# Kernel optimization log

Hardware: AMD Instinct MI355X
Metric: run time of the kernel (lower is better)

## Reference

```python
import jax, jax.numpy as jnp
import numpy as np

B, NN, D, H, L, E, NC = 512, 64, 128, 4, 2, 262144, 8
N = B * NN
HD = D // H


def _mlp(x, W1, b1, W2, b2):
    return jax.nn.relu(x @ W1 + b1) @ W2 + b2


def setup_inputs() -> dict:
    key = jax.random.key(0)
    ks = iter(jax.random.split(key, 64))
    w = lambda shape, s=0.02: jax.random.normal(next(ks), shape, dtype=jnp.float32) * s
    inp = {
        'node_features': jax.random.randint(next(ks), (N,), 0, NC, dtype=jnp.int32),
        'edge_index': jax.random.randint(next(ks), (2, E), 0, N, dtype=jnp.int32),
        'ptr': jnp.arange(B + 1, dtype=jnp.int32) * NN,
        'node_emb_table': w((NC, D), 1.0),
        'edge_emb': jnp.clip(jax.random.normal(next(ks), (1, D), dtype=jnp.float32), -2.0, 2.0),
        'eW1': w((L, 3 * D, D)), 'eb1': jnp.zeros((L, D)), 'eW2': w((L, D, D)), 'eb2': jnp.zeros((L, D)),
        'nW1': w((L, 3 * D, D)), 'nb1': jnp.zeros((L, D)), 'nW2': w((L, D, D)), 'nb2': jnp.zeros((L, D)),
        'gW1': w((L, 3 * D, D)), 'gb1': jnp.zeros((L, D)), 'gW2': w((L, D, D)), 'gb2': jnp.zeros((L, D)),
        'projW': w((D, 3 * D)), 'projb': jnp.zeros((3 * D,)),
        'Wq': w((D, D)), 'Wk': w((D, D)), 'Wv': w((D, D)),
        'bq': jnp.zeros((D,)), 'bk': jnp.zeros((D,)), 'bv': jnp.zeros((D,)),
        'outW': w((D, D)), 'outb': jnp.zeros((D,)),
        'sW1': w((D, D)), 'sb1': jnp.zeros((D,)), 'sW2': w((D, D)), 'sb2': jnp.zeros((D,)),
        'rW1': w((D, D)), 'rb1': jnp.zeros((D,)), 'rW2': w((D, D)), 'rb2': jnp.zeros((D,)),
        'stW1': w((D, D)), 'stb1': jnp.zeros((D,)), 'stW2': w((D, 1)), 'stb2': jnp.zeros((1,)),
        'temperature': jnp.float32(1.0),
    }
    return inp


def reference(node_features, edge_index, ptr, node_emb_table, edge_emb,
              eW1, eb1, eW2, eb2, nW1, nb1, nW2, nb2, gW1, gb1, gW2, gb2,
              projW, projb, Wq, Wk, Wv, bq, bk, bv, outW, outb,
              sW1, sb1, sW2, sb2, rW1, rb1, rW2, rb2,
              stW1, stb1, stW2, stb2, temperature):
    n_graphs = ptr.shape[0] - 1                       # static
    batch_idx = jnp.repeat(jnp.arange(n_graphs), NN)  # uniform graphs of NN nodes
    node_embs = node_emb_table[node_features]         # [N, D]
    edge_embs = jnp.broadcast_to(edge_emb, (edge_index.shape[1], D))  # [E, D]
    g = jnp.zeros((n_graphs, D), node_embs.dtype)
    src, dst = edge_index[0], edge_index[1]
    for l in range(L):
        ein = jnp.concatenate([node_embs[src], node_embs[dst], edge_embs], -1)  # [E, 3D]
        edge_embs = edge_embs + _mlp(ein, eW1[l], eb1[l], eW2[l], eb2[l])
        node_aggr = jax.ops.segment_sum(edge_embs, dst, num_segments=N)         # [N, D]
        nin = jnp.concatenate([node_embs, node_aggr, g[batch_idx]], -1)
        node_embs = node_embs + _mlp(nin, nW1[l], nb1[l], nW2[l], nb2[l])
        eg = jax.ops.segment_sum(node_aggr, batch_idx, num_segments=n_graphs)
        ng = jax.ops.segment_sum(node_embs, batch_idx, num_segments=n_graphs)
        g = g + _mlp(jnp.concatenate([ng, eg, g], -1), gW1[l], gb1[l], gW2[l], gb2[l])
    # projection + self-attention over the NN nodes of each graph
    x = node_embs.reshape(n_graphs, NN, D) @ projW + projb   # [B, NN, 3D]
    q, k, v = jnp.split(x, 3, axis=-1)
    qh = (q @ Wq + bq).reshape(n_graphs, NN, H, HD)
    kh = (k @ Wk + bk).reshape(n_graphs, NN, H, HD)
    vh = (v @ Wv + bv).reshape(n_graphs, NN, H, HD)
    scores = jnp.einsum('bqhd,bkhd->bhqk', qh, kh) / jnp.sqrt(jnp.float32(HD))
    attn = jax.nn.softmax(scores, axis=-1)
    ctx = jnp.einsum('bhqk,bkhd->bqhd', attn, vh).reshape(n_graphs, NN, D)
    a = ctx @ outW + outb
    senders = _mlp(a, sW1, sb1, sW2, sb2)
    receivers = _mlp(a, rW1, rb1, rW2, rb2)
    edge_actions = jnp.einsum('bqd,bkd->bqk', senders, receivers).reshape(n_graphs, NN * NN)
    edge_actions = edge_actions / jax.nn.softplus(temperature)
    stop = _mlp(g, stW1, stb1, stW2, stb2)[:, 0]
    at = jnp.full((n_graphs, 3), -jnp.inf, dtype=edge_actions.dtype)
    at = at.at[:, 1].set(jax.nn.log_sigmoid(-stop))   # ADD_EDGE
    at = at.at[:, 2].set(jax.nn.log_sigmoid(stop))    # EXIT
    return (at, edge_actions)
```

## Files before the change

### kernel.cpp

```cpp
#include <hip/hip_runtime.h>
#include <hip/hip_bf16.h>
#include <cstdint>
#include <cstddef>

#define D_   128
#define NN_  64
#define B_   512
#define N_   32768
#define E_   262144

typedef float4 f4;
typedef _Float16 h16;
typedef __attribute__((ext_vector_type(8))) _Float16 h16x8;
typedef __attribute__((ext_vector_type(4))) float f32x4;

__device__ __forceinline__ f4 ld4(const float* p) { return *(const f4*)p; }
__device__ __forceinline__ void st4(float* p, f4 v) { *(f4*)p = v; }

__device__ __forceinline__ int swz(int row, int slot) {
  return row * 128 + ((slot ^ (row & 7)) << 3);
}
__device__ __forceinline__ h16x8 pk8(f4 a, f4 b) {
  h16x8 v;
  v[0]=(h16)a.x; v[1]=(h16)a.y; v[2]=(h16)a.z; v[3]=(h16)a.w;
  v[4]=(h16)b.x; v[5]=(h16)b.y; v[6]=(h16)b.z; v[7]=(h16)b.w;
  return v;
}
#define MFMA16(a,b,c) __builtin_amdgcn_mfma_f32_16x16x32_f16((a),(b),(c),0,0,0)

__device__ __forceinline__ void stage_a32(const float* __restrict__ A, h16* A_s, int r0, int tid) {
  int r = tid >> 2, q = tid & 3;
  const float* Ar = A + (size_t)(r0 + r) * 128 + q * 32;
#pragma unroll
  for (int i = 0; i < 4; ++i)
    *(h16x8*)&A_s[swz(r, q * 4 + i)] = pk8(ld4(Ar + i * 8), ld4(Ar + i * 8 + 4));
}
__device__ __forceinline__ void stage_a16(const h16* __restrict__ A, h16* A_s, int r0, int tid) {
  int r = tid >> 2, q = tid & 3;
  const h16* Ar = A + (size_t)(r0 + r) * 128 + q * 32;
#pragma unroll
  for (int i = 0; i < 4; ++i)
    *(h16x8*)&A_s[swz(r, q * 4 + i)] = *(const h16x8*)(Ar + i * 8);
}
__device__ __forceinline__ void bfrag_g(const h16* __restrict__ Bt, int n0, int lq, int lr, h16x8 bf[2][4]) {
#pragma unroll
  for (int nf = 0; nf < 2; ++nf) {
    const h16* row = Bt + (size_t)(n0 + nf * 16 + lr) * 128 + lq * 8;
#pragma unroll
    for (int ks = 0; ks < 4; ++ks)
      bf[nf][ks] = *(const h16x8*)(row + ks * 32);
  }
}
__device__ __forceinline__ void mfma8(const h16* A_s, h16x8 bf[2][4], f32x4 acc[4][2], int lq, int lr) {
#pragma unroll
  for (int mf = 0; mf < 4; ++mf)
#pragma unroll
    for (int ks = 0; ks < 4; ++ks) {
      h16x8 af = *(h16x8*)&A_s[swz(mf * 16 + lr, ks * 4 + lq)];
      acc[mf][0] = MFMA16(af, bf[0][ks], acc[mf][0]);
      acc[mf][1] = MFMA16(af, bf[1][ks], acc[mf][1]);
    }
}
__device__ __forceinline__ void zacc(f32x4 acc[4][2]) {
#pragma unroll
  for (int mf = 0; mf < 4; ++mf) { acc[mf][0] = (f32x4)0.f; acc[mf][1] = (f32x4)0.f; }
}

__global__ __launch_bounds__(256)
void k_embed(const int* __restrict__ nf, const float* __restrict__ tab, float* __restrict__ out) {
  int idx = blockIdx.x * 256 + threadIdx.x;
  int row = idx >> 5, q = idx & 31;
  st4(out + (size_t)row * D_ + q * 4, ld4(tab + (size_t)nf[row] * D_ + q * 4));
}

__global__ __launch_bounds__(256)
void k_zero_cnt(int* __restrict__ cnt) { cnt[blockIdx.x * 256 + threadIdx.x] = 0; }

__global__ __launch_bounds__(256)
void k_hist(const int* __restrict__ dst, int* __restrict__ cnt) {
  atomicAdd(&cnt[dst[blockIdx.x * 256 + threadIdx.x]], 1);
}

__global__ __launch_bounds__(256)
void k_scan(const int* __restrict__ cnt, int* __restrict__ base, int* __restrict__ cursor) {
  __shared__ int sums[256];
  __shared__ int offs[256];
  const int t = threadIdx.x;
  const int start = t * 128;
  int s = 0;
  for (int i = 0; i < 128; ++i) s += cnt[start + i];
  sums[t] = s;
  __syncthreads();
  if (t == 0) { int acc = 0; for (int i = 0; i < 256; ++i) { offs[i] = acc; acc += sums[i]; } }
  __syncthreads();
  int off = offs[t];
  for (int i = 0; i < 128; ++i) { base[start + i] = off; cursor[start + i] = off; off += cnt[start + i]; }
  if (t == 255) base[N_] = off;
}

__global__ __launch_bounds__(256)
void k_scatter(const int* __restrict__ dst, int* __restrict__ cursor, int* __restrict__ eid) {
  int e = blockIdx.x * 256 + threadIdx.x;
  int p = atomicAdd(&cursor[dst[e]], 1);
  eid[p] = e;
}

__global__ __launch_bounds__(256)
void k_aggr(const h16* __restrict__ edgeb, const int* __restrict__ csrB,
            float* __restrict__ aggr) {
  const int node = blockIdx.x * 4 + (threadIdx.x >> 6);
  const int d2 = (threadIdx.x & 63) * 2;
  const int b0 = csrB[node], b1 = csrB[node + 1];
  float s0 = 0.f, s1 = 0.f;
  for (int i = b0; i < b1; ++i) {
    const h16* p = edgeb + (size_t)i * 128 + d2;
    s0 += (float)p[0]; s1 += (float)p[1];
  }
  aggr[(size_t)node * 128 + d2 + 0] = s0;
  aggr[(size_t)node * 128 + d2 + 1] = s1;
}

struct TP { const float* p[32]; };
__global__ __launch_bounds__(256)
void k_w2t(TP tp, h16* __restrict__ dst) {
  __shared__ h16 w_s[128][132];
  const float* S = tp.p[blockIdx.x];
  h16* Dd = dst + (size_t)blockIdx.x * 16384;
  const int t = threadIdx.x, r = t >> 1, hf = t & 1;
  for (int i = 0; i < 64; i += 4) {
    f4 x = ld4(S + r * 128 + hf * 64 + i);
    w_s[r][hf*64+i+0] = (h16)x.x; w_s[r][hf*64+i+1] = (h16)x.y;
    w_s[r][hf*64+i+2] = (h16)x.z; w_s[r][hf*64+i+3] = (h16)x.w;
  }
  __syncthreads();
  for (int i8 = 0; i8 < 64; i8 += 8) {
    h16x8 v;
#pragma unroll
    for (int j = 0; j < 8; ++j) v[j] = w_s[hf*64 + i8 + j][r];
    *(h16x8*)(Dd + (size_t)r * 128 + hf * 64 + i8) = v;
  }
}

__global__ __launch_bounds__(256, 2)
void k_weff(const float* __restrict__ projW, const h16* __restrict__ wt_qkv,
            h16* __restrict__ wout) {
  __shared__ h16 A_s[64 * 128];
  const int i = blockIdx.x >> 1, half = blockIdx.x & 1;
  const int r0 = half * 64;
  const int tid = threadIdx.x;
  const int lane = tid & 63, w = tid >> 6;
  const int n0 = w * 32, lq = lane >> 4, lr = lane & 15;
  stage_a16(wt_qkv + (size_t)i * 16384, A_s, r0, tid);
  __syncthreads();
  h16x8 bf[2][4];
#pragma unroll
  for (int nf = 0; nf < 2; ++nf) {
    const int r = n0 + nf * 16 + lr;
    const float* prow = projW + (size_t)r * 384 + i * 128 + lq * 8;
#pragma unroll
    for (int ks = 0; ks < 4; ++ks)
      bf[nf][ks] = pk8(ld4(prow + ks * 32), ld4(prow + ks * 32 + 4));
  }
  f32x4 acc[4][2];
  zacc(acc);
  mfma8(A_s, bf, acc, lq, lr);
  h16* Wo = wout + (size_t)i * 16384;
#pragma unroll
  for (int nf = 0; nf < 2; ++nf) {
    const int r = n0 + nf * 16 + lr;
#pragma unroll
    for (int mf = 0; mf < 4; ++mf)
#pragma unroll
      for (int reg = 0; reg < 4; ++reg)
        Wo[(size_t)(r0 + mf * 16 + lq * 4 + reg) * 128 + r] = (h16)acc[mf][nf][reg];
  }
}

__global__ __launch_bounds__(256, 2)
void k_gemm3o(const float* __restrict__ A,
              const h16* __restrict__ B1, const h16* __restrict__ B2,
              const h16* __restrict__ B3,
              const float* __restrict__ bias,
              h16* __restrict__ O1, h16* __restrict__ O2, h16* __restrict__ O3) {
  __shared__ h16 A_s[64 * 128];
  const int tid = threadIdx.x;
  const int r0 = blockIdx.x * 64;
  const int lane = tid & 63, w = tid >> 6;
  const int n0 = w * 32, lq = lane >> 4, lr = lane & 15;
  stage_a32(A, A_s, r0, tid);
  __syncthreads();
  const h16* Bs[3] = {B1, B2, B3};
  h16*       Os[3] = {O1, O2, O3};
#pragma unroll
  for (int o = 0; o < 3; ++o) {
    if (!Bs[o]) break;
    h16x8 bf[2][4];
    f32x4 acc[4][2];
    bfrag_g(Bs[o], n0, lq, lr, bf);
    zacc(acc);
    mfma8(A_s, bf, acc, lq, lr);
#pragma unroll
    for (int nf = 0; nf < 2; ++nf) {
      const int col = n0 + nf * 16 + lr;
      const float bv = bias ? bias[o * 128 + col] : 0.f;
#pragma unroll
      for (int mf = 0; mf < 4; ++mf)
#pragma unroll
        for (int reg = 0; reg < 4; ++reg)
          Os[o][(size_t)(r0 + mf * 16 + lq * 4 + reg) * 128 + col] = (h16)(acc[mf][nf][reg] + bv);
    }
  }
}

__global__ __launch_bounds__(256, 2)
void k_mlp2(const float* __restrict__ A1, const float* __restrict__ A2,
            const float* __restrict__ A3,
            const h16* __restrict__ B1a, const h16* __restrict__ B1b,
            const h16* __restrict__ B1c,
            const float* __restrict__ bias1,
            const h16* __restrict__ B2, const float* __restrict__ bias2,
            const float* __restrict__ addC,
            float* __restrict__ C) {
  __shared__ h16 A_s[64 * 128];
  const int tid = threadIdx.x;
  const int r0 = blockIdx.x * 64;
  const int lane = tid & 63, w = tid >> 6;
  const int n0 = w * 32, lq = lane >> 4, lr = lane & 15;
  h16x8 bf[2][4];
  f32x4 acc[4][2];
  zacc(acc);
  stage_a32(A1, A_s, r0, tid);
  __syncthreads();
  bfrag_g(B1a, n0, lq, lr, bf);
  mfma8(A_s, bf, acc, lq, lr);
  if (A2) {
    __syncthreads();
    stage_a32(A2, A_s, r0, tid);
    __syncthreads();
    bfrag_g(B1b, n0, lq, lr, bf);
    mfma8(A_s, bf, acc, lq, lr);
  }
  if (A3) {
    __syncthreads();
    stage_a32(A3, A_s, r0, tid);
    __syncthreads();
    bfrag_g(B1c, n0, lq, lr, bf);
    mfma8(A_s, bf, acc, lq, lr);
  }
  __syncthreads();
#pragma unroll
  for (int nf = 0; nf < 2; ++nf) {
    const int col = n0 + nf * 16 + lr;
    const float b1v = bias1 ? bias1[col] : 0.f;
#pragma unroll
    for (int mf = 0; mf < 4; ++mf)
#pragma unroll
      for (int reg = 0; reg < 4; ++reg) {
        const int row = mf * 16 + lq * 4 + reg;
        A_s[swz(row, col >> 3) + (col & 7)] = (h16)fmaxf(acc[mf][nf][reg] + b1v, 0.f);
      }
  }
  __syncthreads();
  bfrag_g(B2, n0, lq, lr, bf);
  zacc(acc);
  mfma8(A_s, bf, acc, lq, lr);
#pragma unroll
  for (int nf = 0; nf < 2; ++nf) {
    const int col = n0 + nf * 16 + lr;
    const float b2v = bias2 ? bias2[col] : 0.f;
#pragma unroll
    for (int mf = 0; mf < 4; ++mf)
#pragma unroll
      for (int reg = 0; reg < 4; ++reg) {
        const int row = r0 + mf * 16 + lq * 4 + reg;
        float x = acc[mf][nf][reg] + b2v;
        if (addC) x += addC[(size_t)row * 128 + col];
        C[(size_t)row * 128 + col] = x;
      }
  }
}

__global__ __launch_bounds__(256, 2)
void k_nodemlp(float* __restrict__ node, const float* __restrict__ aggr,
               const float* __restrict__ gbuf,
               const h16* __restrict__ B1a, const h16* __restrict__ B1b,
               const float* __restrict__ nW1c, const float* __restrict__ nb1,
               const h16* __restrict__ B2, const float* __restrict__ nb2,
               float* __restrict__ ngb, float* __restrict__ egb) {
  __shared__ h16 A_s[64 * 128];
  __shared__ float gt_s[2][128];
  __shared__ float eg_s[2][128];
  const int tid = threadIdx.x, g = blockIdx.x, r0 = g * 64;
  const int lane = tid & 63, w = tid >> 6;
  const int n0 = w * 32, lq = lane >> 4, lr = lane & 15;
  h16x8 bf[2][4];
  f32x4 acc[4][2];
  zacc(acc);
  stage_a32(node, A_s, r0, tid);
  __syncthreads();
  bfrag_g(B1a, n0, lq, lr, bf);
  mfma8(A_s, bf, acc, lq, lr);
  {
    const int col = tid & 127, half = tid >> 7;
    float s = 0.f;
    const float* gb = gbuf + (size_t)g * 128;
    for (int j = half * 64; j < half * 64 + 64; ++j)
      s += gb[j] * nW1c[(size_t)j * 128 + col];
    gt_s[half][col] = s;
  }
  __syncthreads();
  stage_a32(aggr, A_s, r0, tid);
  __syncthreads();
  bfrag_g(B1b, n0, lq, lr, bf);
  mfma8(A_s, bf, acc, lq, lr);
  {
    const int col = tid & 127, half = tid >> 7;
    float s = 0.f;
    for (int r = half * 32; r < half * 32 + 32; ++r)
      s += aggr[((size_t)r0 + r) * 128 + col];
    eg_s[half][col] = s;
  }
  __syncthreads();
#pragma unroll
  for (int nf = 0; nf < 2; ++nf) {
    const int col = n0 + nf * 16 + lr;
    const float gt = gt_s[0][col] + gt_s[1][col] + nb1[col];
#pragma unroll
    for (int mf = 0; mf < 4; ++mf)
#pragma unroll
      for (int reg = 0; reg < 4; ++reg) {
        const int row = mf * 16 + lq * 4 + reg;
        A_s[swz(row, col >> 3) + (col & 7)] = (h16)fmaxf(acc[mf][nf][reg] + gt, 0.f);
      }
  }
  if (tid < 128) egb[(size_t)g * 128 + tid] = eg_s[0][tid] + eg_s[1][tid];
  __syncthreads();
  bfrag_g(B2, n0, lq, lr, bf);
  zacc(acc);
  mfma8(A_s, bf, acc, lq, lr);
#pragma unroll
  for (int nf = 0; nf < 2; ++nf) {
    const int col = n0 + nf * 16 + lr;
    const float b2v = nb2[col];
    float cs = 0.f;
#pragma unroll
    for (int mf = 0; mf < 4; ++mf)
#pragma unroll
      for (int reg = 0; reg < 4; ++reg) {
        const int row = r0 + mf * 16 + lq * 4 + reg;
        float x = acc[mf][nf][reg] + b2v + node[(size_t)row * 128 + col];
        node[(size_t)row * 128 + col] = x;
        cs += x;
      }
    cs += __shfl_xor(cs, 16);
    cs += __shfl_xor(cs, 32);
    if (lq == 0) ngb[(size_t)g * 128 + col] = cs;
  }
}

__global__ __launch_bounds__(128)
void k_hc0(const float* __restrict__ ee, const float* __restrict__ W1c,
           const float* __restrict__ b1, float* __restrict__ hc0) {
  int j = threadIdx.x;
  float s = b1[j];
  for (int d = 0; d < 128; ++d) s += ee[d] * W1c[d * 128 + j];
  hc0[j] = s;
}

__global__ __launch_bounds__(256, 2)
void k_edge0(const int* __restrict__ src, const int* __restrict__ dst,
             const int* __restrict__ eid,
             const h16* __restrict__ hs, const h16* __restrict__ hd,
             const float* __restrict__ hc0, const h16* __restrict__ Wt2,
             const float* __restrict__ eb2, const float* __restrict__ ee,
             h16* __restrict__ edgeb) {
  __shared__ h16 H_s[64 * 128];
  __shared__ int ss[64], sd[64];
  const int tid = threadIdx.x;
  const int e0 = blockIdx.x * 64;
  const int lane = tid & 63, w = tid >> 6;
  const int n0 = w * 32, lq = lane >> 4, lr = lane & 15;
  if (tid < 64) { int e = eid[e0 + tid]; ss[tid] = src[e]; sd[tid] = dst[e]; }
  __syncthreads();
  {
    int e = tid >> 2, q = tid & 3;
    const h16* ps = hs + (size_t)ss[e] * 128 + q * 32;
    const h16* pd = hd + (size_t)sd[e] * 128 + q * 32;
#pragma unroll
    for (int i = 0; i < 4; ++i) {
      h16x8 a = *(const h16x8*)(ps + i * 8);
      h16x8 b = *(const h16x8*)(pd + i * 8);
      f4 c0 = ld4(hc0 + q * 32 + i * 8), c1 = ld4(hc0 + q * 32 + i * 8 + 4);
      h16x8 v;
      v[0]=(h16)fmaxf((float)a[0]+(float)b[0]+c0.x,0.f); v[1]=(h16)fmaxf((float)a[1]+(float)b[1]+c0.y,0.f);
      v[2]=(h16)fmaxf((float)a[2]+(float)b[2]+c0.z,0.f); v[3]=(h16)fmaxf((float)a[3]+(float)b[3]+c0.w,0.f);
      v[4]=(h16)fmaxf((float)a[4]+(float)b[4]+c1.x,0.f); v[5]=(h16)fmaxf((float)a[5]+(float)b[5]+c1.y,0.f);
      v[6]=(h16)fmaxf((float)a[6]+(float)b[6]+c1.z,0.f); v[7]=(h16)fmaxf((float)a[7]+(float)b[7]+c1.w,0.f);
      *(h16x8*)&H_s[swz(e, q * 4 + i)] = v;
    }
  }
  __syncthreads();
  h16x8 bf[2][4];
  f32x4 acc[4][2];
  bfrag_g(Wt2, n0, lq, lr, bf);
  zacc(acc);
  mfma8(H_s, bf, acc, lq, lr);
  __syncthreads();
#pragma unroll
  for (int nf = 0; nf < 2; ++nf) {
    const int col = n0 + nf * 16 + lr;
    const float base = eb2[col] + ee[col];
#pragma unroll
    for (int mf = 0; mf < 4; ++mf)
#pragma unroll
      for (int reg = 0; reg < 4; ++reg) {
        const int row = mf * 16 + lq * 4 + reg;
        H_s[swz(row, col >> 3) + (col & 7)] = (h16)(acc[mf][nf][reg] + base);
      }
  }
  __syncthreads();
  {
    int r = tid >> 2, q = tid & 3;
#pragma unroll
    for (int i = 0; i < 4; ++i) {
      int slot = q * 4 + i;
      h16x8 v = *(const h16x8*)&H_s[swz(r, slot)];
      *(h16x8*)(edgeb + (size_t)(e0 + r) * 128 + slot * 8) = v;
    }
  }
}

__global__ __launch_bounds__(256, 2)
void k_edge1(const int* __restrict__ src, const int* __restrict__ dst,
             const int* __restrict__ eid,
             h16* __restrict__ edgeb,
             const h16* __restrict__ hs, const h16* __restrict__ hd,
             const h16* __restrict__ Wt1c, const float* __restrict__ b1,
             const h16* __restrict__ Wt2, const float* __restrict__ b2) {
  __shared__ h16 T_s[64 * 128];
  __shared__ h16 HS_s[64 * 128];
  __shared__ int ss[64], sd[64];
  const int tid = threadIdx.x;
  const int e0 = blockIdx.x * 64;
  const int lane = tid & 63, w = tid >> 6;
  const int n0 = w * 32, lq = lane >> 4, lr = lane & 15;
  if (tid < 64) { int e = eid[e0 + tid]; ss[tid] = src[e]; sd[tid] = dst[e]; }
  {
    int r = tid >> 2, q = tid & 3;
    const h16* Er = edgeb + (size_t)(e0 + r) * 128 + q * 32;
#pragma unroll
    for (int i = 0; i < 4; ++i)
      *(h16x8*)&T_s[swz(r, q * 4 + i)] = *(const h16x8*)(Er + i * 8);
  }
  __syncthreads();
  {
    int e = tid >> 2, q = tid & 3;
    const h16* ps = hs + (size_t)ss[e] * 128 + q * 32;
    const h16* pd = hd + (size_t)sd[e] * 128 + q * 32;
#pragma unroll
    for (int i = 0; i < 4; ++i) {
      h16x8 a = *(const h16x8*)(ps + i * 8);
      h16x8 b = *(const h16x8*)(pd + i * 8);
      f4 c0 = ld4(b1 + q * 32 + i * 8), c1 = ld4(b1 + q * 32 + i * 8 + 4);
      h16x8 v;
      v[0]=(h16)((float)a[0]+(float)b[0]+c0.x); v[1]=(h16)((float)a[1]+(float)b[1]+c0.y);
      v[2]=(h16)((float)a[2]+(float)b[2]+c0.z); v[3]=(h16)((float)a[3]+(float)b[3]+c0.w);
      v[4]=(h16)((float)a[4]+(float)b[4]+c1.x); v[5]=(h16)((float)a[5]+(float)b[5]+c1.y);
      v[6]=(h16)((float)a[6]+(float)b[6]+c1.z); v[7]=(h16)((float)a[7]+(float)b[7]+c1.w);
      *(h16x8*)&HS_s[swz(e, q * 4 + i)] = v;
    }
  }
  h16x8 bf[2][4];
  f32x4 acc[4][2];
  bfrag_g(Wt1c, n0, lq, lr, bf);
  zacc(acc);
  mfma8(T_s, bf, acc, lq, lr);
  float rres[2][4][4];
#pragma unroll
  for (int nf = 0; nf < 2; ++nf) {
    const int col = n0 + nf * 16 + lr;
#pragma unroll
    for (int mf = 0; mf < 4; ++mf)
#pragma unroll
      for (int reg = 0; reg < 4; ++reg) {
        const int row = mf * 16 + lq * 4 + reg;
        rres[nf][mf][reg] = (float)T_s[swz(row, col >> 3) + (col & 7)];
      }
  }
  __syncthreads();
#pragma unroll
  for (int nf = 0; nf < 2; ++nf) {
    const int col = n0 + nf * 16 + lr;
#pragma unroll
    for (int mf = 0; mf < 4; ++mf)
#pragma unroll
      for (int reg = 0; reg < 4; ++reg) {
        const int row = mf * 16 + lq * 4 + reg;
        float x = acc[mf][nf][reg] + (float)HS_s[swz(row, col >> 3) + (col & 7)];
        T_s[swz(row, col >> 3) + (col & 7)] = (h16)fmaxf(x, 0.f);
      }
  }
  __syncthreads();
  bfrag_g(Wt2, n0, lq, lr, bf);
  zacc(acc);
  mfma8(T_s, bf, acc, lq, lr);
#pragma unroll
  for (int nf = 0; nf < 2; ++nf) {
    const int col = n0 + nf * 16 + lr;
    const float b2v = b2[col];
#pragma unroll
    for (int mf = 0; mf < 4; ++mf)
#pragma unroll
      for (int reg = 0; reg < 4; ++reg) {
        const int row = mf * 16 + lq * 4 + reg;
        HS_s[swz(row, col >> 3) + (col & 7)] = (h16)(acc[mf][nf][reg] + b2v + rres[nf][mf][reg]);
      }
  }
  __syncthreads();
  {
    int r = tid >> 2, q = tid & 3;
#pragma unroll
    for (int i = 0; i < 4; ++i) {
      int slot = q * 4 + i;
      h16x8 v = *(const h16x8*)&HS_s[swz(r, slot)];
      *(h16x8*)(edgeb + (size_t)(e0 + r) * 128 + slot * 8) = v;
    }
  }
}

__global__ __launch_bounds__(128)
void k_beff(const float* __restrict__ projb,
            const float* __restrict__ Wq, const float* __restrict__ Wk, const float* __restrict__ Wv,
            const float* __restrict__ bq, const float* __restrict__ bk, const float* __restrict__ bv,
            float* __restrict__ beff) {
  int i = blockIdx.x, k = threadIdx.x;
  const float* W = (i == 0) ? Wq : ((i == 1) ? Wk : Wv);
  const float* bb = (i == 0) ? bq : ((i == 1) ? bk : bv);
  float s = bb[k];
  for (int j = 0; j < 128; ++j) s += projb[i * 128 + j] * W[j * 128 + k];
  beff[i * 128 + k] = s;
}

__global__ __launch_bounds__(256, 2)
void k_qkv_attn(const float* __restrict__ node_in,
                const h16* __restrict__ Wq_t, const h16* __restrict__ Wk_t,
                const h16* __restrict__ Wv_t, const float* __restrict__ beff,
                const h16* __restrict__ outWt, const float* __restrict__ outb,
                float* __restrict__ nodeOut) {
  __shared__ h16 A_s[64 * 128];
  __shared__ h16 q_s[64][136];
  __shared__ h16 k_s[64][136];
  __shared__ h16 v_s[64][136];
  const int tid = threadIdx.x, g = blockIdx.x, r0 = g * 64;
  const int lane = tid & 63, w = tid >> 6;
  const int n0 = w * 32, lq = lane >> 4, lr = lane & 15;
  stage_a32(node_in, A_s, r0, tid);
  __syncthreads();
  const h16* Ws[3] = {Wq_t, Wk_t, Wv_t};
#pragma unroll
  for (int o = 0; o < 3; ++o) {
    h16x8 bf[2][4];
    f32x4 acc[4][2];
    bfrag_g(Ws[o], n0, lq, lr, bf);
    zacc(acc);
    mfma8(A_s, bf, acc, lq, lr);
#pragma unroll
    for (int nf = 0; nf < 2; ++nf) {
      const int col = n0 + nf * 16 + lr;
      const float bv = beff[o * 128 + col];
#pragma unroll
      for (int mf = 0; mf < 4; ++mf)
#pragma unroll
        for (int reg = 0; reg < 4; ++reg) {
          const int row = mf * 16 + lq * 4 + reg;
          h16 x = (h16)(acc[mf][nf][reg] + bv);
          if (o == 0) q_s[row][col] = x;
          else if (o == 1) k_s[row][col] = x;
          else v_s[row][col] = x;
        }
    }
  }
  __syncthreads();
  const int co = n0;
  h16x8 qv[4];
#pragma unroll
  for (int j = 0; j < 4; ++j)
    qv[j] = *(const h16x8*)&q_s[lane][co + j * 8];
  float s[64];
  const float scale = 0.17677669529663688f;
#pragma unroll 8
  for (int k = 0; k < 64; ++k) {
    float a = 0.f;
#pragma unroll
    for (int j = 0; j < 4; ++j) {
      h16x8 k8 = *(const h16x8*)&k_s[k][co + j * 8];
#pragma unroll
      for (int t = 0; t < 8; ++t) a += (float)qv[j][t] * (float)k8[t];
    }
    s[k] = a * scale;
  }
  float m = s[0];
#pragma unroll
  for (int k = 1; k < 64; ++k) m = fmaxf(m, s[k]);
  float sum = 0.f;
#pragma unroll
  for (int k = 0; k < 64; ++k) { s[k] = expf(s[k] - m); sum += s[k]; }
  const float inv = 1.f / sum;
  f4 cv[8];
#pragma unroll
  for (int jj = 0; jj < 8; ++jj) cv[jj] = make_float4(0.f, 0.f, 0.f, 0.f);
#pragma unroll 4
  for (int k = 0; k < 64; ++k) {
    float p = s[k];
#pragma unroll
    for (int j = 0; j < 4; ++j) {
      h16x8 v8 = *(const h16x8*)&v_s[k][co + j * 8];
      cv[2*j].x   += p * (float)v8[0]; cv[2*j].y   += p * (float)v8[1];
      cv[2*j].z   += p * (float)v8[2]; cv[2*j].w   += p * (float)v8[3];
      cv[2*j+1].x += p * (float)v8[4]; cv[2*j+1].y += p * (float)v8[5];
      cv[2*j+1].z += p * (float)v8[6]; cv[2*j+1].w += p * (float)v8[7];
    }
  }
#pragma unroll
  for (int jj = 0; jj < 4; ++jj) {
    f4 a = cv[2*jj], b = cv[2*jj+1];
    a.x *= inv; a.y *= inv; a.z *= inv; a.w *= inv;
    b.x *= inv; b.y *= inv; b.z *= inv; b.w *= inv;
    *(h16x8*)&A_s[swz(lane, (co >> 3) + jj)] = pk8(a, b);
  }
  __syncthreads();
  h16x8 bf[2][4];
  f32x4 acc[4][2];
  bfrag_g(outWt, n0, lq, lr, bf);
  zacc(acc);
  mfma8(A_s, bf, acc, lq, lr);
  const size_t base = (size_t)r0 * 128;
#pragma unroll
  for (int nf = 0; nf < 2; ++nf) {
    const int col = n0 + nf * 16 + lr;
    const float bv = outb[col];
#pragma unroll
    for (int mf = 0; mf < 4; ++mf)
#pragma unroll
      for (int reg = 0; reg < 4; ++reg)
        nodeOut[base + (size_t)(mf * 16 + lq * 4 + reg) * 128 + col] = acc[mf][nf][reg] + bv;
  }
}

__global__ __launch_bounds__(256, 2)
void k_sr_edgeact(const float* __restrict__ node_in,
                  const h16* __restrict__ sW1t, const float* __restrict__ sb1,
                  const h16* __restrict__ sW2t, const float* __restrict__ sb2,
                  const h16* __restrict__ rW1t, const float* __restrict__ rb1,
                  const h16* __restrict__ rW2t, const float* __restrict__ rb2,
                  const float* __restrict__ temp, float* __restrict__ out) {
  __shared__ h16 A_s[64 * 128];
  __shared__ h16 H_s[64 * 128];
  __shared__ h16 S_s[64 * 128];
  __shared__ h16 R_s[64][136];
  const int tid = threadIdx.x, g = blockIdx.x, r0 = g * 64;
  const int lane = tid & 63, w = tid >> 6;
  const int n0 = w * 32, lq = lane >> 4, lr = lane & 15;
  stage_a32(node_in, A_s, r0, tid);
  __syncthreads();
  h16x8 bf[2][4];
  f32x4 acc[4][2];
  bfrag_g(sW1t, n0, lq, lr, bf);
  zacc(acc);
  mfma8(A_s, bf, acc, lq, lr);
#pragma unroll
  for (int nf = 0; nf < 2; ++nf) {
    const int col = n0 + nf * 16 + lr;
    const float b1v = sb1[col];
#pragma unroll
    for (int mf = 0; mf < 4; ++mf)
#pragma unroll
      for (int reg = 0; reg < 4; ++reg) {
        const int row = mf * 16 + lq * 4 + reg;
        H_s[swz(row, col >> 3) + (col & 7)] = (h16)fmaxf(acc[mf][nf][reg] + b1v, 0.f);
      }
  }
  __syncthreads();
  bfrag_g(sW2t, n0, lq, lr, bf);
  zacc(acc);
  mfma8(H_s, bf, acc, lq, lr);
#pragma unroll
  for (int nf = 0; nf < 2; ++nf) {
    const int col = n0 + nf * 16 + lr;
    const float b2v = sb2[col];
#pragma unroll
    for (int mf = 0; mf < 4; ++mf)
#pragma unroll
      for (int reg = 0; reg < 4; ++reg) {
        const int row = mf * 16 + lq * 4 + reg;
        S_s[swz(row, col >> 3) + (col & 7)] = (h16)(acc[mf][nf][reg] + b2v);
      }
  }
  __syncthreads();
  bfrag_g(rW1t, n0, lq, lr, bf);
  zacc(acc);
  mfma8(A_s, bf, acc, lq, lr);
#pragma unroll
  for (int nf = 0; nf < 2; ++nf) {
    const int col = n0 + nf * 16 + lr;
    const float b1v = rb1[col];
#pragma unroll
    for (int mf = 0; mf < 4; ++mf)
#pragma unroll
      for (int reg = 0; reg < 4; ++reg) {
        const int row = mf * 16 + lq * 4 + reg;
        H_s[swz(row, col >> 3) + (col & 7)] = (h16)fmaxf(acc[mf][nf][reg] + b1v, 0.f);
      }
  }
  __syncthreads();
  bfrag_g(rW2t, n0, lq, lr, bf);
  zacc(acc);
  mfma8(H_s, bf, acc, lq, lr);
#pragma unroll
  for (int nf = 0; nf < 2; ++nf) {
    const int col = n0 + nf * 16 + lr;
    const float b2v = rb2[col];
#pragma unroll
    for (int mf = 0; mf < 4; ++mf)
#pragma unroll
      for (int reg = 0; reg < 4; ++reg) {
        const int row = mf * 16 + lq * 4 + reg;
        R_s[row][col] = (h16)(acc[mf][nf][reg] + b2v);
      }
  }
  __syncthreads();
  const int n0e = w * 16;
  h16x8 bfR[4];
#pragma unroll
  for (int ks = 0; ks < 4; ++ks)
    bfR[ks] = *(const h16x8*)&R_s[n0e + lr][lq * 8 + ks * 32];
  f32x4 acc4[4];
#pragma unroll
  for (int mf = 0; mf < 4; ++mf) acc4[mf] = (f32x4)0.f;
#pragma unroll
  for (int mf = 0; mf < 4; ++mf)
#pragma unroll
    for (int ks = 0; ks < 4; ++ks) {
      h16x8 af = *(h16x8*)&S_s[swz(mf * 16 + lr, ks * 4 + lq)];
      acc4[mf] = MFMA16(af, bfR[ks], acc4[mf]);
    }
  const float inv = 1.f / log1pf(expf(temp[0]));
  __syncthreads();
  float* O_s = (float*)H_s;
#pragma unroll
  for (int mf = 0; mf < 4; ++mf)
#pragma unroll
    for (int reg = 0; reg < 4; ++reg)
      O_s[(mf * 16 + lq * 4 + reg) * 64 + n0e + lr] = acc4[mf][reg] * inv;
  __syncthreads();
#pragma unroll
  for (int i = 0; i < 4; ++i)
    st4(out + (size_t)g * 4096 + tid * 16 + i * 4, *(const f4*)&O_s[tid * 16 + i * 4]);
}

__global__ __launch_bounds__(256, 2)
void k_stophead(const float* __restrict__ gbuf, const h16* __restrict__ stW1t,
                const float* __restrict__ stb1, const float* __restrict__ stW2,
                const float* __restrict__ stb2, float* __restrict__ out) {
  __shared__ h16 A_s[64 * 128];
  __shared__ h16 H_s[64 * 128];
  const int tid = threadIdx.x, r0 = blockIdx.x * 64;
  const int lane = tid & 63, w = tid >> 6;
  const int n0 = w * 32, lq = lane >> 4, lr = lane & 15;
  stage_a32(gbuf, A_s, r0, tid);
  __syncthreads();
  h16x8 bf[2][4];
  f32x4 acc[4][2];
  bfrag_g(stW1t, n0, lq, lr, bf);
  zacc(acc);
  mfma8(A_s, bf, acc, lq, lr);
#pragma unroll
  for (int nf = 0; nf < 2; ++nf) {
    const int col = n0 + nf * 16 + lr;
    const float b1v = stb1[col];
#pragma unroll
    for (int mf = 0; mf < 4; ++mf)
#pragma unroll
      for (int reg = 0; reg < 4; ++reg) {
        const int row = mf * 16 + lq * 4 + reg;
        H_s[swz(row, col >> 3) + (col & 7)] = (h16)fmaxf(acc[mf][nf][reg] + b1v, 0.f);
      }
  }
  __syncthreads();
  if (tid < 64) {
    float s = stb2[0];
    for (int c = 0; c < 128; ++c)
      s += (float)H_s[swz(tid, c >> 3) + (c & 7)] * stW2[c];
    float l = log1pf(expf(-fabsf(s)));
    int b = r0 + tid;
    out[b * 3 + 0] = -3.3895313892515355e38f;
    out[b * 3 + 1] = fminf(-s, 0.f) - l;
    out[b * 3 + 2] = fminf(s, 0.f) - l;
  }
}

static const size_t OFF_NODE  = 0;
static const size_t OFF_HSRC  = 4194304;
static const size_t OFF_HDST  = 8388608;
static const size_t OFF_AGGR  = 12582912;
static const size_t OFF_G     = 20971520;
static const size_t OFF_NG    = OFF_G + 65536;
static const size_t OFF_EG    = OFF_NG + 65536;
static const size_t OFF_BEFF  = OFF_EG + 65536;
static const size_t OFF_HC0   = OFF_BEFF + 384;
static const size_t OFF_EDGE  = 21495808;
static const size_t OFF_CSR   = OFF_EDGE + (size_t)E_ * 128;
static const size_t CSR_INTS  = (size_t)N_ + (N_ + 1) + N_ + E_;
static const size_t OFF_WT    = OFF_CSR + ((CSR_INTS + 63) & ~(size_t)63) / 1 / 4 * 4 + 64;

#define WT_WQ 0
#define WT_WK 1
#define WT_WV 2
#define WT_OUTW 3
#define WT_SW1 4
#define WT_SW2 5
#define WT_RW1 6
#define WT_RW2 7
#define WT_STW1 8
#define WT_L(l,i) (9 + (l)*11 + (i))
#define WT_EW1C1 31
#define WT_WEFF 32
#define WTP(i) (wt + (size_t)(i) * 16384)

extern "C" void kernel_launch(void* const* d_in, const int* in_sizes, int n_in,
                              void* d_out, int out_size, void* d_ws, size_t ws_size,
                              hipStream_t stream) {
  (void)in_sizes; (void)n_in; (void)out_size; (void)ws_size;
  const int*   nf    = (const int*)d_in[0];
  const int*   ei    = (const int*)d_in[1];
  const float* tab   = (const float*)d_in[3];
  const float* ee    = (const float*)d_in[4];
  const float* eW1   = (const float*)d_in[5];
  const float* eb1   = (const float*)d_in[6];
  const float* eW2   = (const float*)d_in[7];
  const float* eb2   = (const float*)d_in[8];
  const float* nW1   = (const float*)d_in[9];
  const float* nb1   = (const float*)d_in[10];
  const float* nW2   = (const float*)d_in[11];
  const float* nb2   = (const float*)d_in[12];
  const float* gW1   = (const float*)d_in[13];
  const float* gb1   = (const float*)d_in[14];
  const float* gW2   = (const float*)d_in[15];
  const float* gb2   = (const float*)d_in[16];
  const float* projW = (const float*)d_in[17];
  const float* projb = (const float*)d_in[18];
  const float* Wq    = (const float*)d_in[19];
  const float* Wk    = (const float*)d_in[20];
  const float* Wv    = (const float*)d_in[21];
  const float* bq    = (const float*)d_in[22];
  const float* bk    = (const float*)d_in[23];
  const float* bv    = (const float*)d_in[24];
  const float* outW  = (const float*)d_in[25];
  const float* outb  = (const float*)d_in[26];
  const float* sW1   = (const float*)d_in[27];
  const float* sb1   = (const float*)d_in[28];
  const float* sW2   = (const float*)d_in[29];
  const float* sb2   = (const float*)d_in[30];
  const float* rW1   = (const float*)d_in[31];
  const float* rb1   = (const float*)d_in[32];
  const float* rW2   = (const float*)d_in[33];
  const float* rb2   = (const float*)d_in[34];
  const float* stW1  = (const float*)d_in[35];
  const float* stb1  = (const float*)d_in[36];
  const float* stW2  = (const float*)d_in[37];
  const float* stb2  = (const float*)d_in[38];
  const float* temp  = (const float*)d_in[39];

  const int* srcI = ei;
  const int* dstI = ei + E_;

  float* ws    = (float*)d_ws;
  float* node  = ws + OFF_NODE;
  float* hsrcF = ws + OFF_HSRC;
  float* hdstF = ws + OFF_HDST;
  float* aggr  = ws + OFF_AGGR;
  float* gbuf  = ws + OFF_G;
  float* ngb   = ws + OFF_NG;
  float* egb   = ws + OFF_EG;
  float* beff  = ws + OFF_BEFF;
  float* hc0   = ws + OFF_HC0;
  h16*  hsrcH  = (h16*)hsrcF;
  h16*  hdstH  = (h16*)hdstF;
  h16*  edgebH = (h16*)(ws + OFF_EDGE);
  int* cnt    = (int*)(ws + OFF_CSR);
  int* csrB   = cnt + N_;
  int* cursor = csrB + (N_ + 1);
  int* eidL   = cursor + N_;
  h16* wt     = (h16*)(ws + OFF_WT);
  float* outp = (float*)d_out;

  hipMemsetAsync(gbuf, 0, (size_t)B_ * D_ * sizeof(float), stream);
  k_embed<<<4096, 256, 0, stream>>>(nf, tab, node);

  k_zero_cnt<<<N_ / 256, 256, 0, stream>>>(cnt);
  k_hist<<<E_ / 256, 256, 0, stream>>>(dstI, cnt);
  k_scan<<<1, 256, 0, stream>>>(cnt, csrB, cursor);
  k_scatter<<<E_ / 256, 256, 0, stream>>>(dstI, cursor, eidL);

  TP tp;
  tp.p[WT_WQ] = Wq; tp.p[WT_WK] = Wk; tp.p[WT_WV] = Wv; tp.p[WT_OUTW] = outW;
  tp.p[WT_SW1] = sW1; tp.p[WT_SW2] = sW2; tp.p[WT_RW1] = rW1; tp.p[WT_RW2] = rW2;
  tp.p[WT_STW1] = stW1;
  for (int l = 0; l < 2; ++l) {
    tp.p[WT_L(l,0)]  = eW1 + (size_t)l * 384 * 128;
    tp.p[WT_L(l,1)]  = eW1 + (size_t)l * 384 * 128 + 128 * 128;
    tp.p[WT_L(l,2)]  = eW2 + (size_t)l * 128 * 128;
    tp.p[WT_L(l,3)]  = nW1 + (size_t)l * 384 * 128;
    tp.p[WT_L(l,4)]  = nW1 + (size_t)l * 384 * 128 + 128 * 128;
    tp.p[WT_L(l,5)]  = nW1 + (size_t)l * 384 * 128 + 256 * 128;
    tp.p[WT_L(l,6)]  = nW2 + (size_t)l * 128 * 128;
    tp.p[WT_L(l,7)]  = gW1 + (size_t)l * 384 * 128;
    tp.p[WT_L(l,8)]  = gW1 + (size_t)l * 384 * 128 + 128 * 128;
    tp.p[WT_L(l,9)]  = gW1 + (size_t)l * 384 * 128 + 256 * 128;
    tp.p[WT_L(l,10)] = gW2 + (size_t)l * 128 * 128;
  }
  tp.p[WT_EW1C1] = eW1 + (size_t)384 * 128 + 256 * 128;
  k_w2t<<<32, 256, 0, stream>>>(tp, wt);

  k_weff<<<6, 256, 0, stream>>>(projW, WTP(WT_WQ), WTP(WT_WEFF));
  k_beff<<<3, 128, 0, stream>>>(projb, Wq, Wk, Wv, bq, bk, bv, beff);

  for (int l = 0; l < 2; ++l) {
    const float* eb1l = eb1 + l * 128;
    const float* eb2l = eb2 + l * 128;
    const float* nb1l = nb1 + l * 128;
    const float* nb2l = nb2 + l * 128;
    const float* gb1l = gb1 + l * 128;
    const float* gb2l = gb2 + l * 128;
    const float* nW1cl = nW1 + (size_t)l * 384 * 128 + 256 * 128;

    k_gemm3o<<<N_ / 64, 256, 0, stream>>>(node, WTP(WT_L(l,0)), WTP(WT_L(l,1)), nullptr,
                                          nullptr, hsrcH, hdstH, nullptr);
    if (l == 0) {
      k_hc0<<<1, 128, 0, stream>>>(ee, eW1 + 256 * 128, eb1l, hc0);
      k_edge0<<<E_ / 64, 256, 0, stream>>>(srcI, dstI, eidL, hsrcH, hdstH, hc0,
                                           WTP(WT_L(0,2)), eb2l, ee, edgebH);
    } else {
      k_edge1<<<E_ / 64, 256, 0, stream>>>(srcI, dstI, eidL, edgebH, hsrcH, hdstH,
                                           WTP(WT_EW1C1), eb1l, WTP(WT_L(1,2)), eb2l);
    }
    k_aggr<<<N_ / 4, 256, 0, stream>>>(edgebH, csrB, aggr);
    k_nodemlp<<<B_, 256, 0, stream>>>(node, aggr, gbuf,
                                      WTP(WT_L(l,3)), WTP(WT_L(l,4)),
                                      nW1cl, nb1l,
                                      WTP(WT_L(l,6)), nb2l, ngb, egb);
    k_mlp2<<<B_ / 64, 256, 0, stream>>>(ngb, egb, gbuf,
                                        WTP(WT_L(l,7)), WTP(WT_L(l,8)), WTP(WT_L(l,9)),
                                        gb1l,
                                        WTP(WT_L(l,10)), gb2l, gbuf, gbuf);
  }

  k_qkv_attn<<<B_, 256, 0, stream>>>(node, WTP(WT_WEFF + 0), WTP(WT_WEFF + 1),
                                     WTP(WT_WEFF + 2), beff, WTP(WT_OUTW), outb, node);
  k_sr_edgeact<<<B_, 256, 0, stream>>>(node,
                                       WTP(WT_SW1), sb1, WTP(WT_SW2), sb2,
                                       WTP(WT_RW1), rb1, WTP(WT_RW2), rb2,
                                       temp, outp + 3 * B_);
  k_stophead<<<B_ / 64, 256, 0, stream>>>(gbuf, WTP(WT_STW1), stb1, stW2, stb2, outp);
}
```

Measured before the change: 431.0 us.

## Fuse global MLP into node MLP kernel and merge attention with sender/receiver heads

Result: slower. 442.4 us (+2.6%).

```diff
diff --git a/kernel.cpp b/kernel.cpp
--- a/kernel.cpp
+++ b/kernel.cpp
@@ -213,83 +213,19 @@
 }
 
 __global__ __launch_bounds__(256, 2)
-void k_mlp2(const float* __restrict__ A1, const float* __restrict__ A2,
-            const float* __restrict__ A3,
-            const h16* __restrict__ B1a, const h16* __restrict__ B1b,
-            const h16* __restrict__ B1c,
-            const float* __restrict__ bias1,
-            const h16* __restrict__ B2, const float* __restrict__ bias2,
-            const float* __restrict__ addC,
-            float* __restrict__ C) {
-  __shared__ h16 A_s[64 * 128];
-  const int tid = threadIdx.x;
-  const int r0 = blockIdx.x * 64;
-  const int lane = tid & 63, w = tid >> 6;
-  const int n0 = w * 32, lq = lane >> 4, lr = lane & 15;
-  h16x8 bf[2][4];
-  f32x4 acc[4][2];
-  zacc(acc);
-  stage_a32(A1, A_s, r0, tid);
-  __syncthreads();
-  bfrag_g(B1a, n0, lq, lr, bf);
-  mfma8(A_s, bf, acc, lq, lr);
-  if (A2) {
-    __syncthreads();
-    stage_a32(A2, A_s, r0, tid);
-    __syncthreads();
-    bfrag_g(B1b, n0, lq, lr, bf);
-    mfma8(A_s, bf, acc, lq, lr);
-  }
-  if (A3) {
-    __syncthreads();
-    stage_a32(A3, A_s, r0, tid);
-    __syncthreads();
-    bfrag_g(B1c, n0, lq, lr, bf);
-    mfma8(A_s, bf, acc, lq, lr);
-  }
-  __syncthreads();
-#pragma unroll
-  for (int nf = 0; nf < 2; ++nf) {
-    const int col = n0 + nf * 16 + lr;
-    const float b1v = bias1 ? bias1[col] : 0.f;
-#pragma unroll
-    for (int mf = 0; mf < 4; ++mf)
-#pragma unroll
-      for (int reg = 0; reg < 4; ++reg) {
-        const int row = mf * 16 + lq * 4 + reg;
-        A_s[swz(row, col >> 3) + (col & 7)] = (h16)fmaxf(acc[mf][nf][reg] + b1v, 0.f);
-      }
-  }
-  __syncthreads();
-  bfrag_g(B2, n0, lq, lr, bf);
-  zacc(acc);
-  mfma8(A_s, bf, acc, lq, lr);
-#pragma unroll
-  for (int nf = 0; nf < 2; ++nf) {
-    const int col = n0 + nf * 16 + lr;
-    const float b2v = bias2 ? bias2[col] : 0.f;
-#pragma unroll
-    for (int mf = 0; mf < 4; ++mf)
-#pragma unroll
-      for (int reg = 0; reg < 4; ++reg) {
-        const int row = r0 + mf * 16 + lq * 4 + reg;
-        float x = acc[mf][nf][reg] + b2v;
-        if (addC) x += addC[(size_t)row * 128 + col];
-        C[(size_t)row * 128 + col] = x;
-      }
-  }
-}
-
-__global__ __launch_bounds__(256, 2)
 void k_nodemlp(float* __restrict__ node, const float* __restrict__ aggr,
-               const float* __restrict__ gbuf,
+               float* __restrict__ gbuf,
                const h16* __restrict__ B1a, const h16* __restrict__ B1b,
                const float* __restrict__ nW1c, const float* __restrict__ nb1,
                const h16* __restrict__ B2, const float* __restrict__ nb2,
-               float* __restrict__ ngb, float* __restrict__ egb) {
+               const h16* __restrict__ gW1at, const h16* __restrict__ gW1bt,
+               const h16* __restrict__ gW1ct, const float* __restrict__ gb1,
+               const h16* __restrict__ gW2t, const float* __restrict__ gb2) {
   __shared__ h16 A_s[64 * 128];
   __shared__ float gt_s[2][128];
   __shared__ float eg_s[2][128];
+  __shared__ float ng_s[128];
+  __shared__ float gh_s[128];
   const int tid = threadIdx.x, g = blockIdx.x, r0 = g * 64;
   const int lane = tid & 63, w = tid >> 6;
   const int n0 = w * 32, lq = lane >> 4, lr = lane & 15;
@@ -333,7 +269,6 @@
         A_s[swz(row, col >> 3) + (col & 7)] = (h16)fmaxf(acc[mf][nf][reg] + gt, 0.f);
       }
   }
-  if (tid < 128) egb[(size_t)g * 128 + tid] = eg_s[0][tid] + eg_s[1][tid];
   __syncthreads();
   bfrag_g(B2, n0, lq, lr, bf);
   zacc(acc);
@@ -354,8 +289,35 @@
       }
     cs += __shfl_xor(cs, 16);
     cs += __shfl_xor(cs, 32);
-    if (lq == 0) ngb[(size_t)g * 128 + col] = cs;
-  }
+    if (lq == 0) ng_s[col] = cs;
+  }
+  __syncthreads();
+  if (tid < 128) eg_s[0][tid] += eg_s[1][tid];
+  __syncthreads();
+  const int col = tid & 127, half = tid >> 7;
+  const float* gb_old = gbuf + (size_t)g * 128;
+  {
+    float s = 0.f;
+    const h16* wa = gW1at + (size_t)col * 128;
+    const h16* wb = gW1bt + (size_t)col * 128;
+    const h16* wc = gW1ct + (size_t)col * 128;
+    for (int j = half * 64; j < half * 64 + 64; ++j)
+      s += ng_s[j] * (float)wa[j] + eg_s[0][j] * (float)wb[j] + gb_old[j] * (float)wc[j];
+    gt_s[half][col] = s;
+  }
+  __syncthreads();
+  if (tid < 128) gh_s[tid] = fmaxf(gt_s[0][tid] + gt_s[1][tid] + gb1[tid], 0.f);
+  __syncthreads();
+  {
+    float s = 0.f;
+    const h16* w2 = gW2t + (size_t)col * 128;
+    for (int j = half * 64; j < half * 64 + 64; ++j)
+      s += gh_s[j] * (float)w2[j];
+    gt_s[half][col] = s;
+  }
+  __syncthreads();
+  if (tid < 128)
+    gbuf[(size_t)g * 128 + tid] = gt_s[0][tid] + gt_s[1][tid] + gb2[tid] + gb_old[tid];
 }
 
 __global__ __launch_bounds__(128)
@@ -542,11 +504,15 @@
 }
 
 __global__ __launch_bounds__(256, 2)
-void k_qkv_attn(const float* __restrict__ node_in,
-                const h16* __restrict__ Wq_t, const h16* __restrict__ Wk_t,
-                const h16* __restrict__ Wv_t, const float* __restrict__ beff,
-                const h16* __restrict__ outWt, const float* __restrict__ outb,
-                float* __restrict__ nodeOut) {
+void k_heads(const float* __restrict__ node_in,
+             const h16* __restrict__ Wq_t, const h16* __restrict__ Wk_t,
+             const h16* __restrict__ Wv_t, const float* __restrict__ beff,
+             const h16* __restrict__ outWt, const float* __restrict__ outb,
+             const h16* __restrict__ sW1t, const float* __restrict__ sb1,
+             const h16* __restrict__ sW2t, const float* __restrict__ sb2,
+             const h16* __restrict__ rW1t, const float* __restrict__ rb1,
+             const h16* __restrict__ rW2t, const float* __restrict__ rb2,
+             const float* __restrict__ temp, float* __restrict__ out) {
   __shared__ h16 A_s[64 * 128];
   __shared__ h16 q_s[64][136];
   __shared__ h16 k_s[64][136];
@@ -554,6 +520,8 @@
   const int tid = threadIdx.x, g = blockIdx.x, r0 = g * 64;
   const int lane = tid & 63, w = tid >> 6;
   const int n0 = w * 32, lq = lane >> 4, lr = lane & 15;
+  h16* a_s = &q_s[0][0];
+  h16* h_s = &k_s[0][0];
   stage_a32(node_in, A_s, r0, tid);
   __syncthreads();
   const h16* Ws[3] = {Wq_t, Wk_t, Wv_t};
@@ -582,51 +550,54 @@
   }
   __syncthreads();
   const int co = n0;
-  h16x8 qv[4];
-#pragma unroll
-  for (int j = 0; j < 4; ++j)
-    qv[j] = *(const h16x8*)&q_s[lane][co + j * 8];
-  float s[64];
-  const float scale = 0.17677669529663688f;
+  {
+    h16x8 qv[4];
+#pragma unroll
+    for (int j = 0; j < 4; ++j)
+      qv[j] = *(const h16x8*)&q_s[lane][co + j * 8];
+    float s[64];
+    const float scale = 0.17677669529663688f;
 #pragma unroll 8
-  for (int k = 0; k < 64; ++k) {
-    float a = 0.f;
-#pragma unroll
-    for (int j = 0; j < 4; ++j) {
-      h16x8 k8 = *(const h16x8*)&k_s[k][co + j * 8];
-#pragma unroll
-      for (int t = 0; t < 8; ++t) a += (float)qv[j][t] * (float)k8[t];
-    }
-    s[k] = a * scale;
-  }
-  float m = s[0];
-#pragma unroll
-  for (int k = 1; k < 64; ++k) m = fmaxf(m, s[k]);
-  float sum = 0.f;
-#pragma unroll
-  for (int k = 0; k < 64; ++k) { s[k] = expf(s[k] - m); sum += s[k]; }
-  const float inv = 1.f / sum;
-  f4 cv[8];
-#pragma unroll
-  for (int jj = 0; jj < 8; ++jj) cv[jj] = make_float4(0.f, 0.f, 0.f, 0.f);
+    for (int k = 0; k < 64; ++k) {
+      float a = 0.f;
+#pragma unroll
+      for (int j = 0; j < 4; ++j) {
+        h16x8 k8 = *(const h16x8*)&k_s[k][co + j * 8];
+#pragma unroll
+        for (int t = 0; t < 8; ++t) a += (float)qv[j][t] * (float)k8[t];
+      }
+      s[k] = a * scale;
+    }
+    float m = s[0];
+#pragma unroll
+    for (int k = 1; k < 64; ++k) m = fmaxf(m, s[k]);
+    float sum = 0.f;
+#pragma unroll
+    for (int k = 0; k < 64; ++k) { s[k] = expf(s[k] - m); sum += s[k]; }
+    const float inv = 1.f / sum;
+    f4 cv[8];
+#pragma unroll
+    for (int jj = 0; jj < 8; ++jj) cv[jj] = make_float4(0.f, 0.f, 0.f, 0.f);
 #pragma unroll 4
-  for (int k = 0; k < 64; ++k) {
-    float p = s[k];
-#pragma unroll
-    for (int j = 0; j < 4; ++j) {
-      h16x8 v8 = *(const h16x8*)&v_s[k][co + j * 8];
-      cv[2*j].x   += p * (float)v8[0]; cv[2*j].y   += p * (float)v8[1];
-      cv[2*j].z   += p * (float)v8[2]; cv[2*j].w   += p * (float)v8[3];
-      cv[2*j+1].x += p * (float)v8[4]; cv[2*j+1].y += p * (float)v8[5];
-      cv[2*j+1].z += p * (float)v8[6]; cv[2*j+1].w += p * (float)v8[7];
-    }
-  }
-#pragma unroll
-  for (int jj = 0; jj < 4; ++jj) {
-    f4 a = cv[2*jj], b = cv[2*jj+1];
-    a.x *= inv; a.y *= inv; a.z *= inv; a.w *= inv;
-    b.x *= inv; b.y *= inv; b.z *= inv; b.w *= inv;
-    *(h16x8*)&A_s[swz(lane, (co >> 3) + jj)] = pk8(a, b);
+    for (int k = 0; k < 64; ++k) {
+      float p = s[k];
+#pragma unroll
+      for (int j = 0; j < 4; ++j) {
+        h16x8 v8 = *(const h16x8*)&v_s[k][co + j * 8];
+        cv[2*j].x   += p * (float)v8[0]; cv[2*j].y   += p * (float)v8[1];
+        cv[2*j].z   += p * (float)v8[2]; cv[2*j].w   += p * (float)v8[3];
+        cv[2*j+1].x += p * (float)v8[4]; cv[2*j+1].y += p * (float)v8[5];
+        cv[2*j+1].z += p * (float)v8[6]; cv[2*j+1].w += p * (float)v8[7];
+      }
+    }
+    __syncthreads();
+#pragma unroll
+    for (int jj = 0; jj < 4; ++jj) {
+      f4 a = cv[2*jj], b = cv[2*jj+1];
+      a.x *= inv; a.y *= inv; a.z *= inv; a.w *= inv;
+      b.x *= inv; b.y *= inv; b.z *= inv; b.w *= inv;
+      *(h16x8*)&A_s[swz(lane, (co >> 3) + jj)] = pk8(a, b);
+    }
   }
   __syncthreads();
   h16x8 bf[2][4];
@@ -634,7 +605,6 @@
   bfrag_g(outWt, n0, lq, lr, bf);
   zacc(acc);
   mfma8(A_s, bf, acc, lq, lr);
-  const size_t base = (size_t)r0 * 128;
 #pragma unroll
   for (int nf = 0; nf < 2; ++nf) {
     const int col = n0 + nf * 16 + lr;
@@ -642,32 +612,15 @@
 #pragma unroll
     for (int mf = 0; mf < 4; ++mf)
 #pragma unroll
-      for (int reg = 0; reg < 4; ++reg)
-        nodeOut[base + (size_t)(mf * 16 + lq * 4 + reg) * 128 + col] = acc[mf][nf][reg] + bv;
-  }
-}
-
-__global__ __launch_bounds__(256, 2)
-void k_sr_edgeact(const float* __restrict__ node_in,
-                  const h16* __restrict__ sW1t, const float* __restrict__ sb1,
-                  const h16* __restrict__ sW2t, const float* __restrict__ sb2,
-                  const h16* __restrict__ rW1t, const float* __restrict__ rb1,
-                  const h16* __restrict__ rW2t, const float* __restrict__ rb2,
-                  const float* __restrict__ temp, float* __restrict__ out) {
-  __shared__ h16 A_s[64 * 128];
-  __shared__ h16 H_s[64 * 128];
-  __shared__ h16 S_s[64 * 128];
-  __shared__ h16 R_s[64][136];
-  const int tid = threadIdx.x, g = blockIdx.x, r0 = g * 64;
-  const int lane = tid & 63, w = tid >> 6;
-  const int n0 = w * 32, lq = lane >> 4, lr = lane & 15;
-  stage_a32(node_in, A_s, r0, tid);
-  __syncthreads();
-  h16x8 bf[2][4];
-  f32x4 acc[4][2];
+      for (int reg = 0; reg < 4; ++reg) {
+        const int row = mf * 16 + lq * 4 + reg;
+        a_s[swz(row, col >> 3) + (col & 7)] = (h16)(acc[mf][nf][reg] + bv);
+      }
+  }
+  __syncthreads();
   bfrag_g(sW1t, n0, lq, lr, bf);
   zacc(acc);
-  mfma8(A_s, bf, acc, lq, lr);
+  mfma8(a_s, bf, acc, lq, lr);
 #pragma unroll
   for (int nf = 0; nf < 2; ++nf) {
     const int col = n0 + nf * 16 + lr;
@@ -677,13 +630,13 @@
 #pragma unroll
       for (int reg = 0; reg < 4; ++reg) {
         const int row = mf * 16 + lq * 4 + reg;
-        H_s[swz(row, col >> 3) + (col & 7)] = (h16)fmaxf(acc[mf][nf][reg] + b1v, 0.f);
+        h_s[swz(row, col >> 3) + (col & 7)] = (h16)fmaxf(acc[mf][nf][reg] + b1v, 0.f);
       }
   }
   __syncthreads();
   bfrag_g(sW2t, n0, lq, lr, bf);
   zacc(acc);
-  mfma8(H_s, bf, acc, lq, lr);
+  mfma8(h_s, bf, acc, lq, lr);
 #pragma unroll
   for (int nf = 0; nf < 2; ++nf) {
     const int col = n0 + nf * 16 + lr;
@@ -693,13 +646,13 @@
 #pragma unroll
       for (int reg = 0; reg < 4; ++reg) {
         const int row = mf * 16 + lq * 4 + reg;
-        S_s[swz(row, col >> 3) + (col & 7)] = (h16)(acc[mf][nf][reg] + b2v);
+        A_s[swz(row, col >> 3) + (col & 7)] = (h16)(acc[mf][nf][reg] + b2v);
       }
   }
   __syncthreads();
   bfrag_g(rW1t, n0, lq, lr, bf);
   zacc(acc);
-  mfma8(A_s, bf, acc, lq, lr);
+  mfma8(a_s, bf, acc, lq, lr);
 #pragma unroll
   for (int nf = 0; nf < 2; ++nf) {
     const int col = n0 + nf * 16 + lr;
@@ -709,13 +662,13 @@
 #pragma unroll
       for (int reg = 0; reg < 4; ++reg) {
         const int row = mf * 16 + lq * 4 + reg;
-        H_s[swz(row, col >> 3) + (col & 7)] = (h16)fmaxf(acc[mf][nf][reg] + b1v, 0.f);
+        h_s[swz(row, col >> 3) + (col & 7)] = (h16)fmaxf(acc[mf][nf][reg] + b1v, 0.f);
       }
   }
   __syncthreads();
   bfrag_g(rW2t, n0, lq, lr, bf);
   zacc(acc);
-  mfma8(H_s, bf, acc, lq, lr);
+  mfma8(h_s, bf, acc, lq, lr);
 #pragma unroll
   for (int nf = 0; nf < 2; ++nf) {
     const int col = n0 + nf * 16 + lr;
@@ -725,7 +678,7 @@
 #pragma unroll
       for (int reg = 0; reg < 4; ++reg) {
         const int row = mf * 16 + lq * 4 + reg;
-        R_s[row][col] = (h16)(acc[mf][nf][reg] + b2v);
+        v_s[row][col] = (h16)(acc[mf][nf][reg] + b2v);
       }
   }
   __syncthreads();
@@ -733,7 +686,7 @@
   h16x8 bfR[4];
 #pragma unroll
   for (int ks = 0; ks < 4; ++ks)
-    bfR[ks] = *(const h16x8*)&R_s[n0e + lr][lq * 8 + ks * 32];
+    bfR[ks] = *(const h16x8*)&v_s[n0e + lr][lq * 8 + ks * 32];
   f32x4 acc4[4];
 #pragma unroll
   for (int mf = 0; mf < 4; ++mf) acc4[mf] = (f32x4)0.f;
@@ -741,17 +694,17 @@
   for (int mf = 0; mf < 4; ++mf)
 #pragma unroll
     for (int ks = 0; ks < 4; ++ks) {
-      h16x8 af = *(h16x8*)&S_s[swz(mf * 16 + lr, ks * 4 + lq)];
+      h16x8 af = *(h16x8*)&A_s[swz(mf * 16 + lr, ks * 4 + lq)];
       acc4[mf] = MFMA16(af, bfR[ks], acc4[mf]);
     }
-  const float inv = 1.f / log1pf(expf(temp[0]));
-  __syncthreads();
-  float* O_s = (float*)H_s;
+  const float inv2 = 1.f / log1pf(expf(temp[0]));
+  __syncthreads();
+  float* O_s = (float*)h_s;
 #pragma unroll
   for (int mf = 0; mf < 4; ++mf)
 #pragma unroll
     for (int reg = 0; reg < 4; ++reg)
-      O_s[(mf * 16 + lq * 4 + reg) * 64 + n0e + lr] = acc4[mf][reg] * inv;
+      O_s[(mf * 16 + lq * 4 + reg) * 64 + n0e + lr] = acc4[mf][reg] * inv2;
   __syncthreads();
 #pragma unroll
   for (int i = 0; i < 4; ++i)
@@ -804,9 +757,7 @@
 static const size_t OFF_HDST  = 8388608;
 static const size_t OFF_AGGR  = 12582912;
 static const size_t OFF_G     = 20971520;
-static const size_t OFF_NG    = OFF_G + 65536;
-static const size_t OFF_EG    = OFF_NG + 65536;
-static const size_t OFF_BEFF  = OFF_EG + 65536;
+static const size_t OFF_BEFF  = OFF_G + 65536;
 static const size_t OFF_HC0   = OFF_BEFF + 384;
 static const size_t OFF_EDGE  = 21495808;
 static const size_t OFF_CSR   = OFF_EDGE + (size_t)E_ * 128;
@@ -880,8 +831,6 @@
   float* hdstF = ws + OFF_HDST;
   float* aggr  = ws + OFF_AGGR;
   float* gbuf  = ws + OFF_G;
-  float* ngb   = ws + OFF_NG;
-  float* egb   = ws + OFF_EG;
   float* beff  = ws + OFF_BEFF;
   float* hc0   = ws + OFF_HC0;
   h16*  hsrcH  = (h16*)hsrcF;
@@ -948,18 +897,15 @@
     k_nodemlp<<<B_, 256, 0, stream>>>(node, aggr, gbuf,
                                       WTP(WT_L(l,3)), WTP(WT_L(l,4)),
                                       nW1cl, nb1l,
-                                      WTP(WT_L(l,6)), nb2l, ngb, egb);
-    k_mlp2<<<B_ / 64, 256, 0, stream>>>(ngb, egb, gbuf,
-                                        WTP(WT_L(l,7)), WTP(WT_L(l,8)), WTP(WT_L(l,9)),
-                                        gb1l,
-                                        WTP(WT_L(l,10)), gb2l, gbuf, gbuf);
-  }
-
-  k_qkv_attn<<<B_, 256, 0, stream>>>(node, WTP(WT_WEFF + 0), WTP(WT_WEFF + 1),
-                                     WTP(WT_WEFF + 2), beff, WTP(WT_OUTW), outb, node);
-  k_sr_edgeact<<<B_, 256, 0, stream>>>(node,
-                                       WTP(WT_SW1), sb1, WTP(WT_SW2), sb2,
-                                       WTP(WT_RW1), rb1, WTP(WT_RW2), rb2,
-                                       temp, outp + 3 * B_);
+                                      WTP(WT_L(l,6)), nb2l,
+                                      WTP(WT_L(l,7)), WTP(WT_L(l,8)), WTP(WT_L(l,9)),
+                                      gb1l, WTP(WT_L(l,10)), gb2l);
+  }
+
+  k_heads<<<B_, 256, 0, stream>>>(node, WTP(WT_WEFF + 0), WTP(WT_WEFF + 1),
+                                  WTP(WT_WEFF + 2), beff, WTP(WT_OUTW), outb,
+                                  WTP(WT_SW1), sb1, WTP(WT_SW2), sb2,
+                                  WTP(WT_RW1), rb1, WTP(WT_RW2), rb2,
+                                  temp, outp + 3 * B_);
   k_stophead<<<B_ / 64, 256, 0, stream>>>(gbuf, WTP(WT_STW1), stb1, stW2, stb2, outp);
 }
```
